# Optimization experiments

Measured on AMD Instinct MI355X. Metric: run time of the kernel, lower is better.

Reference implementation:

```python
import jax, jax.numpy as jnp
import numpy as np
from jax import lax

B, T, IN = 32, 512, 32
SNN, TS, HID, HOR = 128, 4, 128, 96
K = 3
THR = 1.0
EPS = 1e-5


def _spike(x):
    # heaviside: fires when (mem - threshold) > 0
    return (x > 0).astype(x.dtype)


def _lif_scan(xs, beta, thr):
    """snntorch Leaky (reset_mechanism='subtract'): mem_t = beta*mem_{t-1} + x_t - spk_{t-1}*thr; spk_t = H(mem_t - thr).
    xs: (S, B, C); beta: (C,). Returns spikes (S,B,C) and membrane (S,B,C)."""
    def step(carry, x):
        mem, rst = carry
        mem = beta * mem + x - rst * thr
        spk = _spike(mem - thr)
        return (mem, lax.stop_gradient(spk)), (spk, mem)
    z = jnp.zeros(xs.shape[1:], xs.dtype)
    _, (spks, mems) = lax.scan(step, (z, z), xs)
    return spks, mems


def setup_inputs() -> dict:
    key = jax.random.key(0)
    ks = jax.random.split(key, 10)
    def rn(k, shape, scale=0.05):
        return jax.random.normal(k, shape, dtype=jnp.float32) * scale
    return {
        "x": jax.random.normal(ks[0], (B, T, IN), dtype=jnp.float32),
        "conv_w": rn(ks[1], (SNN * TS, IN, K)),
        "conv_b": jnp.zeros((SNN * TS,), jnp.float32),
        "bn1_g": jnp.ones((SNN * TS,), jnp.float32),
        "bn1_b": jnp.zeros((SNN * TS,), jnp.float32),
        "beta1": jnp.full((SNN,), 0.9, jnp.float32),
        "bn2_g": jnp.ones((SNN,), jnp.float32),
        "bn2_b": jnp.zeros((SNN,), jnp.float32),
        "beta2": jnp.full((SNN,), 0.9, jnp.float32),
        "gru_wih": rn(ks[2], (3 * HID, IN + SNN)),
        "gru_whh": rn(ks[3], (3 * HID, HID)),
        "gru_bih": jnp.zeros((3 * HID,), jnp.float32),
        "gru_bhh": jnp.zeros((3 * HID,), jnp.float32),
        "q_w": rn(ks[4], (HID, HID)), "q_b": jnp.zeros((HID,), jnp.float32),
        "k_w": rn(ks[5], (HID, HID)), "k_b": jnp.zeros((HID,), jnp.float32),
        "v_w": rn(ks[6], (HID, HID)), "v_b": jnp.zeros((HID,), jnp.float32),
        "bn3_g": jnp.ones((HID,), jnp.float32),
        "bn3_b": jnp.zeros((HID,), jnp.float32),
        "head_w": rn(ks[7], (HOR, HID)),
        "head_b": jnp.zeros((HOR,), jnp.float32),
    }


def reference(x, conv_w, conv_b, bn1_g, bn1_b, beta1, bn2_g, bn2_b, beta2,
              gru_wih, gru_whh, gru_bih, gru_bhh, q_w, q_b, k_w, k_b, v_w, v_b,
              bn3_g, bn3_b, head_w, head_b):
    beta1 = jnp.clip(beta1, 0.0, 0.99)
    beta2 = jnp.clip(beta2, 0.0, 0.99)
    # --- ConvSpikeEncoder: Conv1d -> BatchNorm1d (training stats) -> LIF scan ---
    h = lax.conv_general_dilated(x.transpose(0, 2, 1), conv_w, (1,), [(K // 2, K // 2)],
                                 dimension_numbers=('NCH', 'OIH', 'NCH'))
    h = h + conv_b[None, :, None]  # (B, SNN*TS, T)
    m = h.mean((0, 2), keepdims=True)
    v = jnp.var(h, (0, 2), keepdims=True)
    h = (h - m) * lax.rsqrt(v + EPS) * bn1_g[None, :, None] + bn1_b[None, :, None]
    # (B, SNN*TS, T) -> (T*TS, B, SNN), step index = t*TS + s
    h = h.transpose(0, 2, 1).reshape(B, T * TS, SNN).transpose(1, 0, 2)
    spk_enc, _ = _lif_scan(h, beta1, THR)  # (T*TS, B, SNN)
    # --- per-step BatchNorm1d over batch dim, then second LIF ---
    m2 = spk_enc.mean(1, keepdims=True)
    v2 = jnp.var(spk_enc, 1, keepdims=True)
    h2 = (spk_enc - m2) * lax.rsqrt(v2 + EPS) * bn2_g + bn2_b
    _, mem_rec = _lif_scan(h2, beta2, THR)  # (T*TS, B, SNN)
    # --- downsample membrane: mean over TS sub-steps ---
    mem_down = mem_rec.transpose(1, 0, 2).reshape(B, T, TS, SNN).mean(2)  # (B, T, SNN)
    hc = jnp.concatenate([x, mem_down], -1)  # (B, T, IN+SNN)
    # --- GRU (PyTorch gate order r,z,n) ---
    def gstep(hprev, xt):
        gi = xt @ gru_wih.T + gru_bih
        gh = hprev @ gru_whh.T + gru_bhh
        ir, iz, inn = jnp.split(gi, 3, -1)
        hr, hz, hn = jnp.split(gh, 3, -1)
        r = jax.nn.sigmoid(ir + hr)
        zg = jax.nn.sigmoid(iz + hz)
        n = jnp.tanh(inn + r * hn)
        hnew = (1.0 - zg) * n + zg * hprev
        return hnew, hnew
    _, gru_seq = lax.scan(gstep, jnp.zeros((B, HID), x.dtype), hc.transpose(1, 0, 2))
    g = gru_seq.transpose(1, 0, 2)  # (B, T, HID)
    # --- SpikingAttention: sigmoid(QK^T*scale) @ V, mean over T, BatchNorm ---
    Q = g @ q_w.T + q_b
    Kk = g @ k_w.T + k_b
    V = g @ v_w.T + v_b
    attn = jax.nn.sigmoid(jnp.einsum('btc,bsc->bts', Q, Kk) * (HID ** -0.5))
    out = jnp.einsum('bts,bsc->btc', attn, V).mean(1)  # (B, HID)
    m3 = out.mean(0, keepdims=True)
    v3 = jnp.var(out, 0, keepdims=True)
    out = (out - m3) * lax.rsqrt(v3 + EPS) * bn3_g + bn3_b
    return out @ head_w.T + head_b  # (B, HOR)
```

## Files before the change

kernel.cpp:

```cpp
#include <hip/hip_runtime.h>
#include <math.h>

#define EPSV 1e-5f

#if __has_builtin(__builtin_amdgcn_exp2f)
#define EXP2F(x) __builtin_amdgcn_exp2f(x)
#else
#define EXP2F(x) exp2f(x)
#endif
#if __has_builtin(__builtin_amdgcn_rcpf)
#define RCPF(x) __builtin_amdgcn_rcpf(x)
#else
#define RCPF(x) (1.0f/(x))
#endif

__device__ __forceinline__ float fsigmoid(float x){
  return RCPF(1.0f + EXP2F(-1.4426950408889634f * x));
}
__device__ __forceinline__ float ftanh(float x){
  return RCPF(0.5f + 0.5f * EXP2F(-2.8853900817779268f * x)) - 1.0f;
}
__device__ __forceinline__ unsigned short f2bf(float f){
  unsigned u = __float_as_uint(f);
  return (unsigned short)((u + 0x7FFFu + ((u >> 16) & 1u)) >> 16);
}

typedef __attribute__((ext_vector_type(8))) short bf16x8;
typedef __attribute__((ext_vector_type(8))) short s16x8;
typedef __attribute__((ext_vector_type(4))) float f32x4;
typedef __attribute__((ext_vector_type(2))) _Float16 f16x2;
typedef __attribute__((ext_vector_type(8))) _Float16 f16x8;

#if __has_builtin(__builtin_amdgcn_fdot2)
#define FDOT2(a,b,c) __builtin_amdgcn_fdot2(a,b,c,false)
#else
__device__ __forceinline__ float FDOT2(f16x2 a, f16x2 b, float c){
  return c + (float)a[0]*(float)b[0] + (float)a[1]*(float)b[1];
}
#endif

__device__ __forceinline__ float dot8(f16x8 w, f16x8 h, float acc){
  f16x2 w0 = {w[0],w[1]}, w1 = {w[2],w[3]}, w2 = {w[4],w[5]}, w3 = {w[6],w[7]};
  f16x2 h0 = {h[0],h[1]}, h1 = {h[2],h[3]}, h2 = {h[4],h[5]}, h3 = {h[6],h[7]};
  acc = FDOT2(w0,h0,acc); acc = FDOT2(w1,h1,acc);
  acc = FDOT2(w2,h2,acc); acc = FDOT2(w3,h3,acc);
  return acc;
}

__global__ __launch_bounds__(256) void k_conv(const float* __restrict__ x, const float* __restrict__ w,
        const float* __restrict__ cb, float* __restrict__ hp, float* __restrict__ s1g, float* __restrict__ s2g,
        unsigned short* __restrict__ x_bf){
  __shared__ float xs[32*321];
  __shared__ float ws[32*97];
  __shared__ float bs[32];
  const int tid = threadIdx.x;
  const int t0 = blockIdx.x * 8;
  const int n0 = blockIdx.y * 8;
  for (int idx = tid; idx < 32*10*32; idx += 256){
    int bq = idx / 320; int rem = idx - bq*320; int tt = rem >> 5; int i = rem & 31;
    int tg = t0 - 1 + tt;
    float v = 0.f;
    if (tg >= 0 && tg < 512) v = x[(bq*512 + tg)*32 + i];
    xs[bq*321 + tt*32 + i] = v;
  }
  for (int idx = tid; idx < 32*96; idx += 256){
    int row = idx / 96; int within = idx - row*96;
    int ss = row >> 3; int nl = row & 7;
    int c = ss*128 + n0 + nl;
    ws[row*97 + within] = w[c*96 + within];
  }
  if (tid < 32){
    int ss = tid >> 3, nl = tid & 7;
    bs[tid] = cb[ss*128 + n0 + nl];
  }
  __syncthreads();
  if (blockIdx.y == 0){
    for (int idx = tid; idx < 32*8*32; idx += 256){
      int bq = idx >> 8; int rem = idx & 255; int tt = rem >> 5; int i = rem & 31;
      x_bf[(bq*512 + t0 + tt)*32 + i] = f2bf(xs[bq*321 + (tt+1)*32 + i]);
    }
  }
  const int b = tid & 31;
  const int nl = tid >> 5;
  float acc[4][8];
  #pragma unroll
  for (int ss = 0; ss < 4; ++ss){
    float bv = bs[ss*8 + nl];
    #pragma unroll
    for (int t = 0; t < 8; ++t) acc[ss][t] = bv;
  }
  for (int i = 0; i < 32; ++i){
    #pragma unroll
    for (int k = 0; k < 3; ++k){
      float w0 = ws[(0*8+nl)*97 + i*3 + k];
      float w1 = ws[(1*8+nl)*97 + i*3 + k];
      float w2 = ws[(2*8+nl)*97 + i*3 + k];
      float w3 = ws[(3*8+nl)*97 + i*3 + k];
      #pragma unroll
      for (int t = 0; t < 8; ++t){
        float xv = xs[b*321 + (t+k)*32 + i];
        acc[0][t] += xv*w0; acc[1][t] += xv*w1; acc[2][t] += xv*w2; acc[3][t] += xv*w3;
      }
    }
  }
  #pragma unroll
  for (int ss = 0; ss < 4; ++ss){
    int n = n0 + nl;
    float s1 = 0.f, s2 = 0.f;
    #pragma unroll
    for (int t = 0; t < 8; ++t){
      float v = acc[ss][t];
      int s = (t0 + t)*4 + ss;
      hp[s*4096 + n*32 + b] = v;
      s1 += v; s2 += v*v;
    }
    #pragma unroll
    for (int off = 1; off < 32; off <<= 1){
      s1 += __shfl_xor(s1, off);
      s2 += __shfl_xor(s2, off);
    }
    if (b == 0){
      int c = ss*128 + n;
      atomicAdd(&s1g[c], s1);
      atomicAdd(&s2g[c], s2);
    }
  }
}

__global__ __launch_bounds__(256) void k_cvt_all(const float* __restrict__ wih,
        const float* __restrict__ qw, const float* __restrict__ kw, const float* __restrict__ vw,
        const float* __restrict__ whh,
        unsigned short* __restrict__ wih_bf, unsigned short* __restrict__ wqkv_bf,
        _Float16* __restrict__ whh_h,
        const float* __restrict__ s1g, const float* __restrict__ s2g,
        const float* __restrict__ g, const float* __restrict__ bb,
        float* __restrict__ a1, float* __restrict__ b1){
  if (blockIdx.x >= 624){
    int c = (blockIdx.x - 624)*256 + threadIdx.x;
    if (c < 512){
      float m = s1g[c] * (1.f/16384.f);
      float v = s2g[c] * (1.f/16384.f) - m*m;
      float sc = g[c] * rsqrtf(v + EPSV);
      a1[c] = sc;
      b1[c] = bb[c] - m*sc;
    }
    return;
  }
  int i = blockIdx.x*256 + threadIdx.x;
  if (i < 61440){ wih_bf[i] = f2bf(wih[i]); return; }
  int r = i - 61440;
  if (r < 16384){ wqkv_bf[r] = f2bf(qw[r]); return; }
  r -= 16384;
  if (r < 16384){ wqkv_bf[16384 + r] = f2bf(kw[r]); return; }
  r -= 16384;
  if (r < 16384){ wqkv_bf[32768 + r] = f2bf(vw[r]); return; }
  r -= 16384;
  if (r < 49152){ whh_h[r] = (_Float16)whh[r]; }
}

__global__ __launch_bounds__(256) void k_lif(const float* __restrict__ hp,
        const float* __restrict__ a1, const float* __restrict__ b1,
        const float* __restrict__ beta1, const float* __restrict__ g2v, const float* __restrict__ b2v,
        const float* __restrict__ beta2, unsigned short* __restrict__ md_t){
  const int tid = threadIdx.x;
  const int b = tid & 31;
  const int n = blockIdx.x * 8 + (tid >> 5);
  float a1r0 = a1[0*128+n], a1r1 = a1[1*128+n], a1r2 = a1[2*128+n], a1r3 = a1[3*128+n];
  float b1r0 = b1[0*128+n], b1r1 = b1[1*128+n], b1r2 = b1[2*128+n], b1r3 = b1[3*128+n];
  float be1 = fminf(fmaxf(beta1[n], 0.f), 0.99f);
  float be2 = fminf(fmaxf(beta2[n], 0.f), 0.99f);
  float g2 = g2v[n], bb2 = b2v[n];
  float m1 = 0.f, r1 = 0.f, m2 = 0.f, r2 = 0.f;
  const float* base = hp + n*32 + b;
  float c0 = base[0], c1 = base[4096], c2 = base[2*4096], c3 = base[3*4096];
  const float* nb1 = base + 16384;
  float d0 = nb1[0], d1 = nb1[4096], d2 = nb1[2*4096], d3 = nb1[3*4096];

#define LIF_STEP(CV, A1R, B1R) { \
    float x1 = CV*A1R + B1R; \
    m1 = be1*m1 + x1 - r1; \
    bool sp = (m1 > 1.0f); \
    unsigned long long mk = __ballot(sp); \
    float spk = sp ? 1.f : 0.f; r1 = spk; \
    unsigned hf = (tid & 32) ? (unsigned)(mk >> 32) : (unsigned)mk; \
    float mean = (float)__popc(hf) * 0.03125f; \
    float var = mean - mean*mean; \
    float h2 = (spk - mean) * rsqrtf(var + EPSV) * g2 + bb2; \
    m2 = be2*m2 + h2 - r2; \
    r2 = (m2 > 1.0f) ? 1.f : 0.f; \
    accd += m2; }

  for (int t = 0; t < 512; ++t){
    float e0 = 0.f, e1 = 0.f, e2 = 0.f, e3 = 0.f;
    if (t < 510){
      const float* nb = base + (size_t)(t+2)*16384;
      e0 = nb[0]; e1 = nb[4096]; e2 = nb[2*4096]; e3 = nb[3*4096];
    }
    float accd = 0.f;
    LIF_STEP(c0, a1r0, b1r0)
    LIF_STEP(c1, a1r1, b1r1)
    LIF_STEP(c2, a1r2, b1r2)
    LIF_STEP(c3, a1r3, b1r3)
    md_t[((t*128) + n)*32 + b] = f2bf(accd * 0.25f);
    c0 = d0; c1 = d1; c2 = d2; c3 = d3;
    d0 = e0; d1 = e1; d2 = e2; d3 = e3;
  }
#undef LIF_STEP
}

__global__ __launch_bounds__(256) void k_tr(const unsigned short* __restrict__ md_t,
        unsigned short* __restrict__ md_bf){
  __shared__ unsigned short l[128][40];
  const int t = blockIdx.x;
  const int tid = threadIdx.x;
  const unsigned short* src = md_t + (size_t)t*4096;
  #pragma unroll
  for (int r = 0; r < 2; ++r){
    int idx = tid*16 + r*8;
    s16x8 v = *(const s16x8*)(src + idx);
    int nn = idx >> 5, b0 = idx & 31;
    #pragma unroll
    for (int e = 0; e < 8; ++e) l[nn][b0 + e] = (unsigned short)v[e];
  }
  __syncthreads();
  const int b = tid >> 3, seg = tid & 7;
  unsigned short tmp[16];
  #pragma unroll
  for (int i = 0; i < 16; ++i) tmp[i] = l[seg*16 + i][b];
  unsigned short* dst = md_bf + (size_t)(b*512 + t)*128 + seg*16;
  *(s16x8*)(dst + 0) = *(s16x8*)&tmp[0];
  *(s16x8*)(dst + 8) = *(s16x8*)&tmp[8];
}

__global__ __launch_bounds__(256) void k_mm_gi(const unsigned short* __restrict__ xbf,
        const unsigned short* __restrict__ mdbf, const unsigned short* __restrict__ wihbf,
        const float* __restrict__ bih, float* __restrict__ gi2){
  const int tid = threadIdx.x;
  const int w = tid >> 6, l = tid & 63;
  const int c16 = l & 15, kg = l >> 4;
  const int m0 = (blockIdx.x*4 + w) * 16;
  const int mrow = m0 + c16;
  bf16x8 a0 = *(const bf16x8*)&xbf[(size_t)mrow*32 + kg*8];
  const unsigned short* mdp = &mdbf[(size_t)mrow*128 + kg*8];
  bf16x8 a1 = *(const bf16x8*)(mdp + 0);
  bf16x8 a2 = *(const bf16x8*)(mdp + 32);
  bf16x8 a3 = *(const bf16x8*)(mdp + 64);
  bf16x8 a4 = *(const bf16x8*)(mdp + 96);
  for (int nt2 = 0; nt2 < 8; ++nt2){
    int n0 = nt2*16;
    const unsigned short* wr = &wihbf[(size_t)(      n0 + c16)*160 + kg*8];
    const unsigned short* wz = &wihbf[(size_t)(128 + n0 + c16)*160 + kg*8];
    const unsigned short* wn = &wihbf[(size_t)(256 + n0 + c16)*160 + kg*8];
    f32x4 ar = {0.f,0.f,0.f,0.f}, az = {0.f,0.f,0.f,0.f}, an = {0.f,0.f,0.f,0.f};
    #pragma unroll
    for (int c = 0; c < 5; ++c){
      bf16x8 br = *(const bf16x8*)(wr + c*32);
      bf16x8 bz = *(const bf16x8*)(wz + c*32);
      bf16x8 bn = *(const bf16x8*)(wn + c*32);
      bf16x8 aa = (c == 0) ? a0 : (c == 1) ? a1 : (c == 2) ? a2 : (c == 3) ? a3 : a4;
      ar = __builtin_amdgcn_mfma_f32_16x16x32_bf16(aa, br, ar, 0, 0, 0);
      az = __builtin_amdgcn_mfma_f32_16x16x32_bf16(aa, bz, az, 0, 0, 0);
      an = __builtin_amdgcn_mfma_f32_16x16x32_bf16(aa, bn, an, 0, 0, 0);
    }
    float br_ = bih[n0 + c16], bz_ = bih[128 + n0 + c16], bn_ = bih[256 + n0 + c16];
    int jj = n0 + c16;
    #pragma unroll
    for (int r = 0; r < 4; ++r){
      float4 o = { ar[r] + br_, az[r] + bz_, an[r] + bn_, 0.f };
      *(float4*)&gi2[(size_t)(m0 + kg*4 + r)*512 + jj*4] = o;
    }
  }
}

template<int SEL>
__device__ __forceinline__ float dpp_qp(float x){
  return __int_as_float(__builtin_amdgcn_mov_dpp(__float_as_int(x), SEL, 0xF, 0xF, true));
}
__device__ __forceinline__ float qbc(float x, int u){
  switch(u){
    case 0: return dpp_qp<0x00>(x);
    case 1: return dpp_qp<0x55>(x);
    case 2: return dpp_qp<0xAA>(x);
    default: return dpp_qp<0xFF>(x);
  }
}
__global__ __launch_bounds__(512, 2) void k_gru(const float* __restrict__ gi2, const _Float16* __restrict__ whh_h,
        const float* __restrict__ bhh, unsigned short* __restrict__ gout_bf){
  const int b = blockIdx.x;
  const int tid = threadIdx.x;
  const int j = tid >> 2;
  const int q = tid & 3;
  __shared__ _Float16 hs[2][144];
  const _Float16* wbr = whh_h + (size_t)(      j)*128 + q*32;
  const _Float16* wbz = whh_h + (size_t)(128 + j)*128 + q*32;
  const _Float16* wbn = whh_h + (size_t)(256 + j)*128 + q*32;
  f16x8 wr0 = *(const f16x8*)(wbr+ 0), wr1 = *(const f16x8*)(wbr+ 8),
        wr2 = *(const f16x8*)(wbr+16), wr3 = *(const f16x8*)(wbr+24);
  f16x8 wz0 = *(const f16x8*)(wbz+ 0), wz1 = *(const f16x8*)(wbz+ 8),
        wz2 = *(const f16x8*)(wbz+16), wz3 = *(const f16x8*)(wbz+24);
  f16x8 wn0 = *(const f16x8*)(wbn+ 0), wn1 = *(const f16x8*)(wbn+ 8),
        wn2 = *(const f16x8*)(wbn+16), wn3 = *(const f16x8*)(wbn+24);
  float bh_r = 0.f, bh_z = 0.f, bh_n = 0.f;
  if (!q){
    bh_r = bhh[j]; bh_z = bhh[128+j]; bh_n = bhh[256+j];
  }
  const float* gib = gi2 + (size_t)b*512*512;
  f32x4 G = *(const f32x4*)(gib + (size_t)q*512 + j*4);
  f32x4 N = *(const f32x4*)(gib + (size_t)(4 + q)*512 + j*4);
  if (tid < 128) hs[0][tid] = (_Float16)0.f;
  float hprev = 0.f;
  __syncthreads();
  for (int g = 0; g < 128; ++g){
    f32x4 N2 = {0.f,0.f,0.f,0.f};
    if (g < 126) N2 = *(const f32x4*)(gib + (size_t)(4*(g+2) + q)*512 + j*4);
    #pragma unroll
    for (int u = 0; u < 4; ++u){
      const int t = g*4 + u;
      float gr = qbc(G[0], u);
      float gz = qbc(G[1], u);
      float gn = qbc(G[2], u);
      const f16x8* hq = (const f16x8*)&hs[t & 1][q*32];
      f16x8 h0 = hq[0], h1 = hq[1], h2 = hq[2], h3 = hq[3];
      float ar = 0.f, az = 0.f, an = 0.f;
      ar = dot8(wr0,h0,ar); ar = dot8(wr1,h1,ar); ar = dot8(wr2,h2,ar); ar = dot8(wr3,h3,ar);
      az = dot8(wz0,h0,az); az = dot8(wz1,h1,az); az = dot8(wz2,h2,az); az = dot8(wz3,h3,az);
      an = dot8(wn0,h0,an); an = dot8(wn1,h1,an); an = dot8(wn2,h2,an); an = dot8(wn3,h3,an);
      ar += dpp_qp<0xB1>(ar); ar += dpp_qp<0x4E>(ar);
      az += dpp_qp<0xB1>(az); az += dpp_qp<0x4E>(az);
      an += dpp_qp<0xB1>(an); an += dpp_qp<0x4E>(an);
      if (!q){
        float r = fsigmoid(gr + ar + bh_r);
        float z = fsigmoid(gz + az + bh_z);
        float nn = ftanh(gn + r*(an + bh_n));
        float hn = (1.f - z)*nn + z*hprev;
        hprev = hn;
        hs[(t + 1) & 1][j] = (_Float16)hn;
        gout_bf[((size_t)b*512 + t)*128 + j] = f2bf(hn);
      }
      __syncthreads();
    }
    G = N; N = N2;
  }
}

__global__ __launch_bounds__(256) void k_mm_qkv(const unsigned short* __restrict__ gbf,
        const unsigned short* __restrict__ wbf, const float* __restrict__ qb2,
        const float* __restrict__ kb2, const float* __restrict__ vb2,
        unsigned short* __restrict__ Qbf, unsigned short* __restrict__ Kbf, float* __restrict__ Vb){
  const int tid = threadIdx.x;
  const int w = tid >> 6, l = tid & 63;
  const int c16 = l & 15, kg = l >> 4;
  const int m0 = (blockIdx.x*4 + w) * 16;
  const unsigned short* gp = &gbf[(size_t)(m0 + c16)*128 + kg*8];
  bf16x8 a0 = *(const bf16x8*)(gp + 0);
  bf16x8 a1 = *(const bf16x8*)(gp + 32);
  bf16x8 a2 = *(const bf16x8*)(gp + 64);
  bf16x8 a3 = *(const bf16x8*)(gp + 96);
  for (int nt = 0; nt < 24; ++nt){
    int n0 = nt*16;
    const unsigned short* wp = &wbf[(size_t)(n0 + c16)*128 + kg*8];
    bf16x8 b0 = *(const bf16x8*)(wp + 0);
    bf16x8 b1 = *(const bf16x8*)(wp + 32);
    bf16x8 b2 = *(const bf16x8*)(wp + 64);
    bf16x8 b3 = *(const bf16x8*)(wp + 96);
    f32x4 acc = {0.f,0.f,0.f,0.f};
    acc = __builtin_amdgcn_mfma_f32_16x16x32_bf16(a0, b0, acc, 0, 0, 0);
    acc = __builtin_amdgcn_mfma_f32_16x16x32_bf16(a1, b1, acc, 0, 0, 0);
    acc = __builtin_amdgcn_mfma_f32_16x16x32_bf16(a2, b2, acc, 0, 0, 0);
    acc = __builtin_amdgcn_mfma_f32_16x16x32_bf16(a3, b3, acc, 0, 0, 0);
    int n = n0 + c16;
    if (n < 128){
      float bias = qb2[n];
      #pragma unroll
      for (int r = 0; r < 4; ++r)
        Qbf[(size_t)(m0 + kg*4 + r)*128 + n] = f2bf(acc[r] + bias);
    } else if (n < 256){
      float bias = kb2[n-128];
      #pragma unroll
      for (int r = 0; r < 4; ++r)
        Kbf[(size_t)(m0 + kg*4 + r)*128 + (n-128)] = f2bf(acc[r] + bias);
    } else {
      float bias = vb2[n-256];
      #pragma unroll
      for (int r = 0; r < 4; ++r)
        Vb[(size_t)(m0 + kg*4 + r)*128 + (n-256)] = acc[r] + bias;
    }
  }
}

__global__ __launch_bounds__(256) void k_attn(const unsigned short* __restrict__ Qbf,
        const unsigned short* __restrict__ Kbf, float* __restrict__ av){
  const int tid = threadIdx.x;
  const int b  = blockIdx.x;
  const int st = blockIdx.y;
  const int w  = tid >> 6;
  const int l  = tid & 63;
  const int c16 = l & 15;
  const int kg  = l >> 4;
  const float SC = 0.08838834764831845f;
  const unsigned short* kp = Kbf + ((size_t)(b*512 + st*64 + w*16 + c16))*128 + kg*8;
  bf16x8 a0 = *(const bf16x8*)(kp + 0);
  bf16x8 a1 = *(const bf16x8*)(kp + 32);
  bf16x8 a2 = *(const bf16x8*)(kp + 64);
  bf16x8 a3 = *(const bf16x8*)(kp + 96);
  const unsigned short* qb = Qbf + ((size_t)(b*512 + c16))*128 + kg*8;
  float ps0 = 0.f, ps1 = 0.f, ps2 = 0.f, ps3 = 0.f;
  for (int tt = 0; tt < 32; ++tt){
    const unsigned short* qp = qb + (size_t)tt*16*128;
    bf16x8 b0 = *(const bf16x8*)(qp + 0);
    bf16x8 b1 = *(const bf16x8*)(qp + 32);
    bf16x8 b2 = *(const bf16x8*)(qp + 64);
    bf16x8 b3 = *(const bf16x8*)(qp + 96);
    f32x4 acc = {0.f, 0.f, 0.f, 0.f};
    acc = __builtin_amdgcn_mfma_f32_16x16x32_bf16(a0, b0, acc, 0, 0, 0);
    acc = __builtin_amdgcn_mfma_f32_16x16x32_bf16(a1, b1, acc, 0, 0, 0);
    acc = __builtin_amdgcn_mfma_f32_16x16x32_bf16(a2, b2, acc, 0, 0, 0);
    acc = __builtin_amdgcn_mfma_f32_16x16x32_bf16(a3, b3, acc, 0, 0, 0);
    ps0 += fsigmoid(acc[0]*SC);
    ps1 += fsigmoid(acc[1]*SC);
    ps2 += fsigmoid(acc[2]*SC);
    ps3 += fsigmoid(acc[3]*SC);
  }
  #pragma unroll
  for (int off = 1; off < 16; off <<= 1){
    ps0 += __shfl_xor(ps0, off);
    ps1 += __shfl_xor(ps1, off);
    ps2 += __shfl_xor(ps2, off);
    ps3 += __shfl_xor(ps3, off);
  }
  if (c16 == 0){
    int sb = st*64 + w*16 + kg*4;
    av[b*512 + sb + 0] = ps0 * (1.f/512.f);
    av[b*512 + sb + 1] = ps1 * (1.f/512.f);
    av[b*512 + sb + 2] = ps2 * (1.f/512.f);
    av[b*512 + sb + 3] = ps3 * (1.f/512.f);
  }
}

__global__ __launch_bounds__(128) void k_av(const float* __restrict__ av, const float* __restrict__ Vb,
        float* __restrict__ out0){
  int b = blockIdx.x, c = threadIdx.x;
  float a0 = 0.f, a1 = 0.f, a2 = 0.f, a3 = 0.f;
  for (int s = 0; s < 512; s += 4){
    a0 += av[b*512 + s+0] * Vb[(size_t)(b*512 + s+0)*128 + c];
    a1 += av[b*512 + s+1] * Vb[(size_t)(b*512 + s+1)*128 + c];
    a2 += av[b*512 + s+2] * Vb[(size_t)(b*512 + s+2)*128 + c];
    a3 += av[b*512 + s+3] * Vb[(size_t)(b*512 + s+3)*128 + c];
  }
  out0[b*128 + c] = (a0 + a1) + (a2 + a3);
}

__global__ __launch_bounds__(256) void k_final(const float* __restrict__ out0,
        const float* __restrict__ g3, const float* __restrict__ b3,
        const float* __restrict__ hw, const float* __restrict__ hb, float* __restrict__ out){
  __shared__ float on[32*132];
  const int tid = threadIdx.x;
  if (tid < 128){
    int c = tid;
    float s = 0.f;
    for (int bq = 0; bq < 32; ++bq) s += out0[bq*128 + c];
    float m = s * (1.f/32.f);
    float v = 0.f;
    for (int bq = 0; bq < 32; ++bq){ float d = out0[bq*128 + c] - m; v += d*d; }
    v *= (1.f/32.f);
    float sc = g3[c] * rsqrtf(v + EPSV);
    float sh = b3[c] - m*sc;
    for (int bq = 0; bq < 32; ++bq) on[bq*132 + c] = out0[bq*128 + c]*sc + sh;
  }
  __syncthreads();
  for (int o = tid; o < 32*96; o += 256){
    int bq = o / 96, hh = o - bq*96;
    float acc = hb[hh];
    for (int k = 0; k < 128; ++k) acc += on[bq*132 + k] * hw[hh*128 + k];
    out[o] = acc;
  }
}

extern "C" void kernel_launch(void* const* d_in, const int* in_sizes, int n_in,
                              void* d_out, int out_size, void* d_ws, size_t ws_size,
                              hipStream_t stream){
  const float* x      = (const float*)d_in[0];
  const float* conv_w = (const float*)d_in[1];
  const float* conv_b = (const float*)d_in[2];
  const float* bn1_g  = (const float*)d_in[3];
  const float* bn1_b  = (const float*)d_in[4];
  const float* beta1  = (const float*)d_in[5];
  const float* bn2_g  = (const float*)d_in[6];
  const float* bn2_b  = (const float*)d_in[7];
  const float* beta2  = (const float*)d_in[8];
  const float* g_wih  = (const float*)d_in[9];
  const float* g_whh  = (const float*)d_in[10];
  const float* g_bih  = (const float*)d_in[11];
  const float* g_bhh  = (const float*)d_in[12];
  const float* q_w    = (const float*)d_in[13];
  const float* q_b    = (const float*)d_in[14];
  const float* k_w    = (const float*)d_in[15];
  const float* k_b    = (const float*)d_in[16];
  const float* v_w    = (const float*)d_in[17];
  const float* v_b    = (const float*)d_in[18];
  const float* bn3_g  = (const float*)d_in[19];
  const float* bn3_b  = (const float*)d_in[20];
  const float* head_w = (const float*)d_in[21];
  const float* head_b = (const float*)d_in[22];

  char* ws = (char*)d_ws;
  float* hp            = (float*)ws;
  unsigned short* md_bf= (unsigned short*)(ws + 33554432);
  unsigned short* md_t = (unsigned short*)(ws + 37748736);
  unsigned short* g_bf = (unsigned short*)(ws + 37748736);
  unsigned short* x_bf = (unsigned short*)(ws + 41943040);
  unsigned short* wih_bf  = (unsigned short*)(ws + 42991616);
  unsigned short* wqkv_bf = (unsigned short*)(ws + 43114496);
  _Float16* whh_h      = (_Float16*)(ws + 43212800);
  float* s1g = (float*)(ws + 50331648);
  float* s2g = (float*)(ws + 50331648 + 2048);
  float* a1  = (float*)(ws + 50331648 + 4096);
  float* b1  = (float*)(ws + 50331648 + 6144);
  float* av  = (float*)(ws + 50331648 + 8192);
  float* out0= (float*)(ws + 50331648 + 8192 + 65536);
  float* gi2 = (float*)ws;
  unsigned short* Qbf = (unsigned short*)ws;
  unsigned short* Kbf = (unsigned short*)(ws + 4194304);
  float* Vb  = (float*)(ws + 8388608);

  (void)hipMemsetAsync(ws + 50331648, 0, 4096, stream);

  k_conv<<<dim3(64, 16), 256, 0, stream>>>(x, conv_w, conv_b, hp, s1g, s2g, x_bf);
  k_cvt_all<<<626, 256, 0, stream>>>(g_wih, q_w, k_w, v_w, g_whh, wih_bf, wqkv_bf, whh_h,
                                     s1g, s2g, bn1_g, bn1_b, a1, b1);
  k_lif<<<16, 256, 0, stream>>>(hp, a1, b1, beta1, bn2_g, bn2_b, beta2, md_t);
  k_tr<<<512, 256, 0, stream>>>(md_t, md_bf);
  k_mm_gi<<<256, 256, 0, stream>>>(x_bf, md_bf, wih_bf, g_bih, gi2);
  k_gru<<<32, 512, 0, stream>>>(gi2, whh_h, g_bhh, g_bf);
  k_mm_qkv<<<256, 256, 0, stream>>>(g_bf, wqkv_bf, q_b, k_b, v_b, Qbf, Kbf, Vb);
  k_attn<<<dim3(32, 8), 256, 0, stream>>>(Qbf, Kbf, av);
  k_av<<<32, 128, 0, stream>>>(av, Vb, out0);
  k_final<<<1, 256, 0, stream>>>(out0, bn3_g, bn3_b, head_w, head_b, (float*)d_out);
}
```

Measured before the change: 615.2 us.

## Halve GRU threads per hidden unit and split final head across blocks

```diff
diff --git a/kernel.cpp b/kernel.cpp
--- a/kernel.cpp
+++ b/kernel.cpp
@@ -276,62 +276,69 @@
 __device__ __forceinline__ float dpp_qp(float x){
   return __int_as_float(__builtin_amdgcn_mov_dpp(__float_as_int(x), SEL, 0xF, 0xF, true));
 }
-__device__ __forceinline__ float qbc(float x, int u){
-  switch(u){
-    case 0: return dpp_qp<0x00>(x);
-    case 1: return dpp_qp<0x55>(x);
-    case 2: return dpp_qp<0xAA>(x);
-    default: return dpp_qp<0xFF>(x);
-  }
-}
-__global__ __launch_bounds__(512, 2) void k_gru(const float* __restrict__ gi2, const _Float16* __restrict__ whh_h,
+__global__ __launch_bounds__(256, 1) void k_gru(const float* __restrict__ gi2, const _Float16* __restrict__ whh_h,
         const float* __restrict__ bhh, unsigned short* __restrict__ gout_bf){
   const int b = blockIdx.x;
   const int tid = threadIdx.x;
-  const int j = tid >> 2;
-  const int q = tid & 3;
+  const int j = tid >> 1;
+  const int half = tid & 1;
+  const int k0 = half * 64;
   __shared__ _Float16 hs[2][144];
-  const _Float16* wbr = whh_h + (size_t)(      j)*128 + q*32;
-  const _Float16* wbz = whh_h + (size_t)(128 + j)*128 + q*32;
-  const _Float16* wbn = whh_h + (size_t)(256 + j)*128 + q*32;
-  f16x8 wr0 = *(const f16x8*)(wbr+ 0), wr1 = *(const f16x8*)(wbr+ 8),
-        wr2 = *(const f16x8*)(wbr+16), wr3 = *(const f16x8*)(wbr+24);
-  f16x8 wz0 = *(const f16x8*)(wbz+ 0), wz1 = *(const f16x8*)(wbz+ 8),
-        wz2 = *(const f16x8*)(wbz+16), wz3 = *(const f16x8*)(wbz+24);
-  f16x8 wn0 = *(const f16x8*)(wbn+ 0), wn1 = *(const f16x8*)(wbn+ 8),
-        wn2 = *(const f16x8*)(wbn+16), wn3 = *(const f16x8*)(wbn+24);
+  const _Float16* wbr = whh_h + (size_t)(      j)*128 + k0;
+  const _Float16* wbz = whh_h + (size_t)(128 + j)*128 + k0;
+  const _Float16* wbn = whh_h + (size_t)(256 + j)*128 + k0;
+  f16x8 wr[8], wz[8], wn[8];
+  #pragma unroll
+  for (int i = 0; i < 8; ++i){
+    wr[i] = *(const f16x8*)(wbr + i*8);
+    wz[i] = *(const f16x8*)(wbz + i*8);
+    wn[i] = *(const f16x8*)(wbn + i*8);
+  }
   float bh_r = 0.f, bh_z = 0.f, bh_n = 0.f;
-  if (!q){
+  if (!half){
     bh_r = bhh[j]; bh_z = bhh[128+j]; bh_n = bhh[256+j];
   }
-  const float* gib = gi2 + (size_t)b*512*512;
-  f32x4 G = *(const f32x4*)(gib + (size_t)q*512 + j*4);
-  f32x4 N = *(const f32x4*)(gib + (size_t)(4 + q)*512 + j*4);
+  const float* gib = gi2 + (size_t)b*512*512 + j*4;
+  f32x4 G[4], N[4];
+  #pragma unroll
+  for (int u = 0; u < 4; ++u){
+    G[u] = *(const f32x4*)(gib + (size_t)u*512);
+    N[u] = *(const f32x4*)(gib + (size_t)(4+u)*512);
+  }
   if (tid < 128) hs[0][tid] = (_Float16)0.f;
   float hprev = 0.f;
   __syncthreads();
   for (int g = 0; g < 128; ++g){
-    f32x4 N2 = {0.f,0.f,0.f,0.f};
-    if (g < 126) N2 = *(const f32x4*)(gib + (size_t)(4*(g+2) + q)*512 + j*4);
+    f32x4 N2[4];
+    if (g < 126){
+      #pragma unroll
+      for (int u = 0; u < 4; ++u)
+        N2[u] = *(const f32x4*)(gib + (size_t)(4*(g+2)+u)*512);
+    } else {
+      #pragma unroll
+      for (int u = 0; u < 4; ++u) N2[u] = (f32x4){0.f,0.f,0.f,0.f};
+    }
     #pragma unroll
     for (int u = 0; u < 4; ++u){
       const int t = g*4 + u;
-      float gr = qbc(G[0], u);
-      float gz = qbc(G[1], u);
-      float gn = qbc(G[2], u);
-      const f16x8* hq = (const f16x8*)&hs[t & 1][q*32];
-      f16x8 h0 = hq[0], h1 = hq[1], h2 = hq[2], h3 = hq[3];
-      float ar = 0.f, az = 0.f, an = 0.f;
-      ar = dot8(wr0,h0,ar); ar = dot8(wr1,h1,ar); ar = dot8(wr2,h2,ar); ar = dot8(wr3,h3,ar);
-      az = dot8(wz0,h0,az); az = dot8(wz1,h1,az); az = dot8(wz2,h2,az); az = dot8(wz3,h3,az);
-      an = dot8(wn0,h0,an); an = dot8(wn1,h1,an); an = dot8(wn2,h2,an); an = dot8(wn3,h3,an);
-      ar += dpp_qp<0xB1>(ar); ar += dpp_qp<0x4E>(ar);
-      az += dpp_qp<0xB1>(az); az += dpp_qp<0x4E>(az);
-      an += dpp_qp<0xB1>(an); an += dpp_qp<0x4E>(an);
-      if (!q){
-        float r = fsigmoid(gr + ar + bh_r);
-        float z = fsigmoid(gz + az + bh_z);
-        float nn = ftanh(gn + r*(an + bh_n));
+      const f16x8* hq = (const f16x8*)&hs[t & 1][k0];
+      f16x8 h0 = hq[0], h1 = hq[1], h2 = hq[2], h3 = hq[3],
+            h4 = hq[4], h5 = hq[5], h6 = hq[6], h7 = hq[7];
+      float ar0 = 0.f, ar1 = 0.f, az0 = 0.f, az1 = 0.f, an0 = 0.f, an1 = 0.f;
+      ar0 = dot8(wr[0],h0,ar0); ar0 = dot8(wr[1],h1,ar0); ar0 = dot8(wr[2],h2,ar0); ar0 = dot8(wr[3],h3,ar0);
+      ar1 = dot8(wr[4],h4,ar1); ar1 = dot8(wr[5],h5,ar1); ar1 = dot8(wr[6],h6,ar1); ar1 = dot8(wr[7],h7,ar1);
+      az0 = dot8(wz[0],h0,az0); az0 = dot8(wz[1],h1,az0); az0 = dot8(wz[2],h2,az0); az0 = dot8(wz[3],h3,az0);
+      az1 = dot8(wz[4],h4,az1); az1 = dot8(wz[5],h5,az1); az1 = dot8(wz[6],h6,az1); az1 = dot8(wz[7],h7,az1);
+      an0 = dot8(wn[0],h0,an0); an0 = dot8(wn[1],h1,an0); an0 = dot8(wn[2],h2,an0); an0 = dot8(wn[3],h3,an0);
+      an1 = dot8(wn[4],h4,an1); an1 = dot8(wn[5],h5,an1); an1 = dot8(wn[6],h6,an1); an1 = dot8(wn[7],h7,an1);
+      float ar = ar0 + ar1, az = az0 + az1, an = an0 + an1;
+      ar += dpp_qp<0xB1>(ar);
+      az += dpp_qp<0xB1>(az);
+      an += dpp_qp<0xB1>(an);
+      if (!half){
+        float r = fsigmoid(G[u][0] + ar + bh_r);
+        float z = fsigmoid(G[u][1] + az + bh_z);
+        float nn = ftanh(G[u][2] + r*(an + bh_n));
         float hn = (1.f - z)*nn + z*hprev;
         hprev = hn;
         hs[(t + 1) & 1][j] = (_Float16)hn;
@@ -339,7 +346,8 @@
       }
       __syncthreads();
     }
-    G = N; N = N2;
+    #pragma unroll
+    for (int u = 0; u < 4; ++u){ G[u] = N[u]; N[u] = N2[u]; }
   }
 }
 
@@ -453,26 +461,30 @@
 __global__ __launch_bounds__(256) void k_final(const float* __restrict__ out0,
         const float* __restrict__ g3, const float* __restrict__ b3,
         const float* __restrict__ hw, const float* __restrict__ hb, float* __restrict__ out){
-  __shared__ float on[32*132];
-  const int tid = threadIdx.x;
+  __shared__ float on[2][132];
+  const int tid = threadIdx.x;
+  const int b0 = blockIdx.x * 2;
   if (tid < 128){
     int c = tid;
     float s = 0.f;
+    #pragma unroll 8
     for (int bq = 0; bq < 32; ++bq) s += out0[bq*128 + c];
     float m = s * (1.f/32.f);
     float v = 0.f;
+    #pragma unroll 8
     for (int bq = 0; bq < 32; ++bq){ float d = out0[bq*128 + c] - m; v += d*d; }
     v *= (1.f/32.f);
     float sc = g3[c] * rsqrtf(v + EPSV);
     float sh = b3[c] - m*sc;
-    for (int bq = 0; bq < 32; ++bq) on[bq*132 + c] = out0[bq*128 + c]*sc + sh;
+    on[0][c] = out0[(b0+0)*128 + c]*sc + sh;
+    on[1][c] = out0[(b0+1)*128 + c]*sc + sh;
   }
   __syncthreads();
-  for (int o = tid; o < 32*96; o += 256){
-    int bq = o / 96, hh = o - bq*96;
+  for (int o = tid; o < 2*96; o += 256){
+    int bl = o / 96, hh = o - bl*96;
     float acc = hb[hh];
-    for (int k = 0; k < 128; ++k) acc += on[bq*132 + k] * hw[hh*128 + k];
-    out[o] = acc;
+    for (int k = 0; k < 128; ++k) acc += on[bl][k] * hw[hh*128 + k];
+    out[(b0 + bl)*96 + hh] = acc;
   }
 }
 
@@ -531,9 +543,9 @@
   k_lif<<<16, 256, 0, stream>>>(hp, a1, b1, beta1, bn2_g, bn2_b, beta2, md_t);
   k_tr<<<512, 256, 0, stream>>>(md_t, md_bf);
   k_mm_gi<<<256, 256, 0, stream>>>(x_bf, md_bf, wih_bf, g_bih, gi2);
-  k_gru<<<32, 512, 0, stream>>>(gi2, whh_h, g_bhh, g_bf);
+  k_gru<<<32, 256, 0, stream>>>(gi2, whh_h, g_bhh, g_bf);
   k_mm_qkv<<<256, 256, 0, stream>>>(g_bf, wqkv_bf, q_b, k_b, v_b, Qbf, Kbf, Vb);
   k_attn<<<dim3(32, 8), 256, 0, stream>>>(Qbf, Kbf, av);
   k_av<<<32, 128, 0, stream>>>(av, Vb, out0);
-  k_final<<<1, 256, 0, stream>>>(out0, bn3_g, bn3_b, head_w, head_b, (float*)d_out);
-}
+  k_final<<<16, 256, 0, stream>>>(out0, bn3_g, bn3_b, head_w, head_b, (float*)d_out);
+}
```

Result: faster. 577.4 us (-6.1%).
